# Kernel tuning notes

Measured on AMD Instinct MI355X. Metric: run time of the kernel, lower is better.

The kernel has to match this reference:

```python
import jax, jax.numpy as jnp
import numpy as np

N_NODES = 50000
N_EDGES = 800000
IN_CH, HID_CH, OUT_CH = 100, 128, 47
ORIG_SIZE = 25000


def sage_conv(x, edge_index, w_l, b_l, w_r):
    """PyG-style SAGEConv with mean aggregation.
    out = lin_l(mean_{j in N(i)} x_j) + lin_r(x_i)
    edge_index[0]=source, edge_index[1]=target.
    """
    src, dst = edge_index[0], edge_index[1]
    n = x.shape[0]
    # gather source features, scatter-sum into targets  [N, d]
    agg = jax.ops.segment_sum(x[src], dst, num_segments=n)
    deg = jax.ops.segment_sum(jnp.ones((src.shape[0],), x.dtype), dst, num_segments=n)
    mean = agg / jnp.maximum(deg, 1.0)[:, None]
    return mean @ w_l + b_l + x @ w_r


def setup_inputs() -> dict:
    key = jax.random.key(0)
    ks = jax.random.split(key, 8)
    x = jax.random.normal(ks[0], (N_NODES, IN_CH), dtype=jnp.float32)
    edge_index = jax.random.randint(ks[1], (2, N_EDGES), 0, N_NODES, dtype=jnp.int32)
    s1 = 1.0 / np.sqrt(IN_CH)
    s2 = 1.0 / np.sqrt(HID_CH)
    w1_l = jax.random.uniform(ks[2], (IN_CH, HID_CH), jnp.float32, -s1, s1)
    b1_l = jax.random.uniform(ks[3], (HID_CH,), jnp.float32, -s1, s1)
    w1_r = jax.random.uniform(ks[4], (IN_CH, HID_CH), jnp.float32, -s1, s1)
    w2_l = jax.random.uniform(ks[5], (HID_CH, OUT_CH), jnp.float32, -s2, s2)
    b2_l = jax.random.uniform(ks[6], (OUT_CH,), jnp.float32, -s2, s2)
    w2_r = jax.random.uniform(ks[7], (HID_CH, OUT_CH), jnp.float32, -s2, s2)
    return {"x": x, "edge_index": edge_index, "original_size": ORIG_SIZE,
            "w1_l": w1_l, "b1_l": b1_l, "w1_r": w1_r,
            "w2_l": w2_l, "b2_l": b2_l, "w2_r": w2_r}


def reference(x, edge_index, original_size, w1_l, b1_l, w1_r, w2_l, b2_l, w2_r):
    h = sage_conv(x, edge_index, w1_l, b1_l, w1_r)   # [N, hidden]
    h = sage_conv(h, edge_index, w2_l, b2_l, w2_r)   # [N, out]
    logp = jax.nn.log_softmax(h, axis=1)
    return logp[:original_size]
```

## Files before the change

kernel.cpp:

```cpp
#include <hip/hip_runtime.h>
#include <hip/hip_fp16.h>
#include <math.h>

constexpr int N    = 50000;
constexpr int E    = 800000;
constexpr int CIN  = 100;
constexpr int CH   = 128;
constexpr int COUT = 47;
constexpr int NOUT = 25000;
constexpr int CP   = 48;
constexpr int NB   = (N + 255) / 256;
constexpr int TN   = 128;
constexpr int NT   = (N + TN - 1) / TN;

constexpr int AS  = 72;
constexpr int HS  = 136;
constexpr int W1K = 256;
constexpr int W2K = 128;

constexpr int HB = (E + 255) / 256;
constexpr int CB = (N * CIN / 4 + 255) / 256;
constexpr int PB = 193;

typedef float f32x4 __attribute__((ext_vector_type(4)));
typedef short v8s  __attribute__((ext_vector_type(8)));

__device__ __forceinline__ void bsplit(float f, ushort& h, ushort& l) {
    uint u = __float_as_uint(f);
    h = (ushort)(u >> 16);
    float fh = __uint_as_float(u & 0xffff0000u);
    l = (ushort)(__float_as_uint(f - fh) >> 16);
}

__global__ __launch_bounds__(256) void pre_kernel(
        const int* __restrict__ dst, int* __restrict__ cnt, int* __restrict__ rank,
        const float* __restrict__ x, __half* __restrict__ x16,
        const float* __restrict__ w1l, const float* __restrict__ w1r,
        const float* __restrict__ w2l, const float* __restrict__ w2r,
        const float* __restrict__ b2l,
        ushort* __restrict__ w1T, ushort* __restrict__ w2T,
        float* __restrict__ b2cat) {
    int bid = blockIdx.x, t = threadIdx.x;
    if (bid < HB) {
        int i = bid * 256 + t;
        if (i < E) rank[i] = atomicAdd(&cnt[dst[i]], 1);
    } else if (bid < HB + CB) {
        int i = (bid - HB) * 256 + t;
        if (i < N * CIN / 4) {
            float4 v = ((const float4*)x)[i];
            __half2 h0 = __floats2half2_rn(v.x, v.y);
            __half2 h1 = __floats2half2_rn(v.z, v.w);
            union { __half2 h[2]; uint2 u; } U;
            U.h[0] = h0; U.h[1] = h1;
            ((uint2*)x16)[i] = U.u;
        }
    } else {
        int i = (bid - HB - CB) * 256 + t;
        if (i < 128 * W1K) {
            int n = i >> 8, k = i & 255;
            float v = 0.0f;
            if (k < 100)                    v = w1l[(size_t)k * CH + n];
            else if (k >= 128 && k < 228)   v = w1r[(size_t)(k - 128) * CH + n];
            ushort h, l; bsplit(v, h, l);
            w1T[i] = h; w1T[128 * W1K + i] = l;
        } else if (i < 128 * W1K + 128 * W2K) {
            int j = i - 128 * W1K;
            int n = j >> 7, k = j & 127;
            float v = 0.0f;
            if (n < COUT)                      v = w2l[(size_t)k * COUT + n];
            else if (n >= 64 && n < 64 + COUT) v = w2r[(size_t)k * COUT + (n - 64)];
            ushort h, l; bsplit(v, h, l);
            w2T[j] = h; w2T[128 * W2K + j] = l;
        } else {
            int j = i - (128 * W1K + 128 * W2K);
            if (j < 128) b2cat[j] = (j >= 64 && j < 64 + COUT) ? b2l[j - 64] : 0.0f;
        }
    }
}

__global__ __launch_bounds__(256) void scan_blocks(const int* __restrict__ cnt,
        int* __restrict__ row_ptr, int* __restrict__ blkSum) {
    __shared__ int s[256];
    int t = threadIdx.x;
    int i = blockIdx.x * 256 + t;
    int v = (i < N) ? cnt[i] : 0;
    s[t] = v;
    __syncthreads();
    for (int off = 1; off < 256; off <<= 1) {
        int a = s[t];
        int u = (t >= off) ? s[t - off] : 0;
        __syncthreads();
        s[t] = a + u;
        __syncthreads();
    }
    if (i < N) row_ptr[i] = s[t] - v;
    if (t == 255) blkSum[blockIdx.x] = s[255];
}

__global__ __launch_bounds__(256) void scan_apply(int* __restrict__ row_ptr,
        const int* __restrict__ blkSum) {
    __shared__ int s[256];
    int t = threadIdx.x, bid = blockIdx.x;
    int a = 0;
    for (int j = t; j < bid; j += 256) a += blkSum[j];
    s[t] = a;
    __syncthreads();
    for (int off = 128; off > 0; off >>= 1) {
        if (t < off) s[t] += s[t + off];
        __syncthreads();
    }
    int offset = s[0];
    int i = bid * 256 + t;
    if (i < N) {
        row_ptr[i] += offset;
        if (i == N - 1) row_ptr[N] = E;
    }
}

__global__ void fill_kernel(const int* __restrict__ src, const int* __restrict__ dst,
        const int* __restrict__ rank, const int* __restrict__ row_ptr,
        int* __restrict__ col) {
    int i = blockIdx.x * blockDim.x + threadIdx.x;
    if (i < E) col[row_ptr[dst[i]] + rank[i]] = src[i];
}

__global__ __launch_bounds__(256) void gather1_kernel(const __half* __restrict__ x16,
        const int* __restrict__ row_ptr, const int* __restrict__ col,
        float* __restrict__ agg1) {
    int t = threadIdx.x;
    int n = blockIdx.x * 4 + (t >> 6);
    int l = t & 63, half = l >> 5, li = l & 31;
    int b = row_ptr[n], e = row_ptr[n + 1];
    float inv = 1.0f / (float)max(e - b, 1);
    const uint2* xb = (const uint2*)x16;
    bool act = li < 25;
    float4 s0 = make_float4(0.f, 0.f, 0.f, 0.f);
    float4 s1 = make_float4(0.f, 0.f, 0.f, 0.f);
    float4 s2 = make_float4(0.f, 0.f, 0.f, 0.f);
    float4 s3 = make_float4(0.f, 0.f, 0.f, 0.f);
    union { uint2 u; __half2 h[2]; } U0, U1, U2, U3;
    int j = b + half;
    for (; j + 6 < e; j += 8) {
        int c0 = col[j], c1 = col[j + 2], c2 = col[j + 4], c3 = col[j + 6];
        if (act) {
            U0.u = xb[(size_t)c0 * 25 + li];
            U1.u = xb[(size_t)c1 * 25 + li];
            U2.u = xb[(size_t)c2 * 25 + li];
            U3.u = xb[(size_t)c3 * 25 + li];
            float2 f0a = __half22float2(U0.h[0]), f0b = __half22float2(U0.h[1]);
            float2 f1a = __half22float2(U1.h[0]), f1b = __half22float2(U1.h[1]);
            float2 f2a = __half22float2(U2.h[0]), f2b = __half22float2(U2.h[1]);
            float2 f3a = __half22float2(U3.h[0]), f3b = __half22float2(U3.h[1]);
            s0.x += f0a.x; s0.y += f0a.y; s0.z += f0b.x; s0.w += f0b.y;
            s1.x += f1a.x; s1.y += f1a.y; s1.z += f1b.x; s1.w += f1b.y;
            s2.x += f2a.x; s2.y += f2a.y; s2.z += f2b.x; s2.w += f2b.y;
            s3.x += f3a.x; s3.y += f3a.y; s3.z += f3b.x; s3.w += f3b.y;
        }
    }
    for (; j < e; j += 2) {
        int c0 = col[j];
        if (act) {
            U0.u = xb[(size_t)c0 * 25 + li];
            float2 f0a = __half22float2(U0.h[0]), f0b = __half22float2(U0.h[1]);
            s0.x += f0a.x; s0.y += f0a.y; s0.z += f0b.x; s0.w += f0b.y;
        }
    }
    float4 s = make_float4(s0.x + s1.x + s2.x + s3.x,
                           s0.y + s1.y + s2.y + s3.y,
                           s0.z + s1.z + s2.z + s3.z,
                           s0.w + s1.w + s2.w + s3.w);
    s.x += __shfl_xor(s.x, 32, 64);
    s.y += __shfl_xor(s.y, 32, 64);
    s.z += __shfl_xor(s.z, 32, 64);
    s.w += __shfl_xor(s.w, 32, 64);
    if (half == 0 && act)
        ((float4*)agg1)[(size_t)n * 25 + li] = make_float4(
            s.x * inv, s.y * inv, s.z * inv, s.w * inv);
}

__global__ __launch_bounds__(256) void fused_gemm(
        const float* __restrict__ agg1, const float* __restrict__ x,
        const ushort* __restrict__ w1T, const float* __restrict__ b1l,
        const ushort* __restrict__ w2T, const float* __restrict__ b2cat,
        __half* __restrict__ gsrc16, float* __restrict__ gself) {
    __shared__ __align__(16) uint lds_u[17408];
    ushort* Ah = (ushort*)lds_u;
    ushort* Al = Ah + 128 * AS;
    ushort* Hh = (ushort*)lds_u;
    ushort* Hl = Hh + 128 * HS;

    int t = threadIdx.x;
    int lane = t & 63;
    int wv = __builtin_amdgcn_readfirstlane(t >> 6);
    int nh = wv & 1, chh = wv >> 1;
    int l15 = lane & 15, lg = lane >> 4;
    int base = blockIdx.x * TN;

    const ushort* w1Th = w1T;
    const ushort* w1Tl = w1T + 128 * W1K;
    const ushort* w2Th = w2T;
    const ushort* w2Tl = w2T + 128 * W2K;

    f32x4 acc[4][4];
    #pragma unroll
    for (int nt = 0; nt < 4; ++nt) {
        float bv = b1l[chh * 64 + nt * 16 + l15];
        #pragma unroll
        for (int mt = 0; mt < 4; ++mt)
            acc[mt][nt] = f32x4{bv, bv, bv, bv};
    }

    int srow = t >> 1, sq = t & 1;
    int nmax = N - 1 - base; if (nmax > TN - 1) nmax = TN - 1;
    int srr = srow <= nmax ? srow : nmax;

    float4 rv[8];
    {
        const float4* Fp = (const float4*)(agg1 + (size_t)(base + srr) * CIN);
        int cj0 = sq * 8;
        #pragma unroll
        for (int q = 0; q < 8; ++q) {
            int cj = cj0 + q;
            rv[q] = (cj < 25) ? Fp[cj] : make_float4(0.f, 0.f, 0.f, 0.f);
        }
    }

    for (int c = 0; c < 4; ++c) {
        float4 nv[8];
        if (c < 3) {
            const float* F = (c + 1 < 2) ? agg1 : x;
            const float4* Fp = (const float4*)(F + (size_t)(base + srr) * CIN);
            int cj0 = ((c + 1) & 1) * 16 + sq * 8;
            #pragma unroll
            for (int q = 0; q < 8; ++q) {
                int cj = cj0 + q;
                nv[q] = (cj < 25) ? Fp[cj] : make_float4(0.f, 0.f, 0.f, 0.f);
            }
        }
        #pragma unroll
        for (int q = 0; q < 8; ++q) {
            ushort h0, h1, h2, h3, l0, l1, l2, l3;
            bsplit(rv[q].x, h0, l0); bsplit(rv[q].y, h1, l1);
            bsplit(rv[q].z, h2, l2); bsplit(rv[q].w, h3, l3);
            int di = srow * AS + sq * 32 + q * 4;
            *(uint2*)(Ah + di) = make_uint2((uint)h0 | ((uint)h1 << 16),
                                            (uint)h2 | ((uint)h3 << 16));
            *(uint2*)(Al + di) = make_uint2((uint)l0 | ((uint)l1 << 16),
                                            (uint)l2 | ((uint)l3 << 16));
        }
        __syncthreads();
        #pragma unroll
        for (int ks = 0; ks < 2; ++ks) {
            v8s ahf[4], alf[4];
            #pragma unroll
            for (int mt = 0; mt < 4; ++mt) {
                int row = nh * 64 + mt * 16 + l15;
                int ko = ks * 32 + lg * 8;
                ahf[mt] = *(const v8s*)(Ah + row * AS + ko);
                alf[mt] = *(const v8s*)(Al + row * AS + ko);
            }
            int kg = c * 64 + ks * 32 + lg * 8;
            #pragma unroll
            for (int nt = 0; nt < 4; ++nt) {
                int n = chh * 64 + nt * 16 + l15;
                v8s bhf = *(const v8s*)(w1Th + (size_t)n * W1K + kg);
                v8s blf = *(const v8s*)(w1Tl + (size_t)n * W1K + kg);
                #pragma unroll
                for (int mt = 0; mt < 4; ++mt) {
                    acc[mt][nt] = __builtin_amdgcn_mfma_f32_16x16x32_bf16(
                        ahf[mt], bhf, acc[mt][nt], 0, 0, 0);
                    acc[mt][nt] = __builtin_amdgcn_mfma_f32_16x16x32_bf16(
                        alf[mt], bhf, acc[mt][nt], 0, 0, 0);
                    acc[mt][nt] = __builtin_amdgcn_mfma_f32_16x16x32_bf16(
                        ahf[mt], blf, acc[mt][nt], 0, 0, 0);
                }
            }
        }
        __syncthreads();
        if (c < 3) {
            #pragma unroll
            for (int q = 0; q < 8; ++q) rv[q] = nv[q];
        }
    }

    #pragma unroll
    for (int mt = 0; mt < 4; ++mt) {
        #pragma unroll
        for (int nt = 0; nt < 4; ++nt) {
            int ch = chh * 64 + nt * 16 + l15;
            #pragma unroll
            for (int r = 0; r < 4; ++r) {
                int node = nh * 64 + mt * 16 + lg * 4 + r;
                ushort h, l; bsplit(acc[mt][nt][r], h, l);
                Hh[node * HS + ch] = h;
                Hl[node * HS + ch] = l;
            }
        }
    }
    __syncthreads();

    bool skip = (chh == 1) && (base >= NOUT);
    if (!skip) {
        #pragma unroll
        for (int nt = 0; nt < 4; ++nt) {
            float bv = b2cat[chh * 64 + nt * 16 + l15];
            #pragma unroll
            for (int mt = 0; mt < 4; ++mt)
                acc[mt][nt] = f32x4{bv, bv, bv, bv};
        }
        #pragma unroll
        for (int ks = 0; ks < 4; ++ks) {
            v8s ahf[4], alf[4];
            #pragma unroll
            for (int mt = 0; mt < 4; ++mt) {
                int node = nh * 64 + mt * 16 + l15;
                int ko = ks * 32 + lg * 8;
                ahf[mt] = *(const v8s*)(Hh + node * HS + ko);
                alf[mt] = *(const v8s*)(Hl + node * HS + ko);
            }
            int kg = ks * 32 + lg * 8;
            #pragma unroll
            for (int nt = 0; nt < 4; ++nt) {
                int n = chh * 64 + nt * 16 + l15;
                v8s bhf = *(const v8s*)(w2Th + (size_t)n * W2K + kg);
                v8s blf = *(const v8s*)(w2Tl + (size_t)n * W2K + kg);
                #pragma unroll
                for (int mt = 0; mt < 4; ++mt) {
                    acc[mt][nt] = __builtin_amdgcn_mfma_f32_16x16x32_bf16(
                        ahf[mt], bhf, acc[mt][nt], 0, 0, 0);
                    acc[mt][nt] = __builtin_amdgcn_mfma_f32_16x16x32_bf16(
                        alf[mt], bhf, acc[mt][nt], 0, 0, 0);
                    acc[mt][nt] = __builtin_amdgcn_mfma_f32_16x16x32_bf16(
                        ahf[mt], blf, acc[mt][nt], 0, 0, 0);
                }
            }
        }
        int lim = chh ? NOUT : N;
        #pragma unroll
        for (int nt = 0; nt < 3; ++nt) {
            int colc = nt * 16 + l15;
            #pragma unroll
            for (int mt = 0; mt < 4; ++mt) {
                #pragma unroll
                for (int r = 0; r < 4; ++r) {
                    int node = base + nh * 64 + mt * 16 + lg * 4 + r;
                    if (node < lim) {
                        if (chh) gself[(size_t)node * CP + colc] = acc[mt][nt][r];
                        else gsrc16[(size_t)node * CP + colc] =
                                 __float2half(acc[mt][nt][r]);
                    }
                }
            }
        }
    }
}

__global__ __launch_bounds__(256) void final_kernel(const __half* __restrict__ gsrc16,
        const float* __restrict__ gself, const int* __restrict__ row_ptr,
        const int* __restrict__ col, float* __restrict__ out) {
    int t = threadIdx.x;
    int n = blockIdx.x * 4 + (t >> 6);
    int c = t & 63;
    int b = row_ptr[n], e = row_ptr[n + 1];
    float inv = 1.0f / (float)max(e - b, 1);
    float a0 = 0.f, a1 = 0.f, a2 = 0.f, a3 = 0.f;
    if (c < CP) {
        int j = b;
        for (; j + 3 < e; j += 4) {
            a0 += __half2float(gsrc16[(size_t)col[j]     * CP + c]);
            a1 += __half2float(gsrc16[(size_t)col[j + 1] * CP + c]);
            a2 += __half2float(gsrc16[(size_t)col[j + 2] * CP + c]);
            a3 += __half2float(gsrc16[(size_t)col[j + 3] * CP + c]);
        }
        for (; j < e; ++j) a0 += __half2float(gsrc16[(size_t)col[j] * CP + c]);
    }
    float val = (c < COUT)
        ? (((a0 + a1) + (a2 + a3)) * inv + gself[(size_t)n * CP + c]) : -INFINITY;
    float m = val;
    #pragma unroll
    for (int off = 32; off > 0; off >>= 1) m = fmaxf(m, __shfl_xor(m, off, 64));
    float ex = (c < COUT) ? expf(val - m) : 0.f;
    float ssum = ex;
    #pragma unroll
    for (int off = 32; off > 0; off >>= 1) ssum += __shfl_xor(ssum, off, 64);
    if (c < COUT)
        __builtin_nontemporal_store(val - m - logf(ssum),
                                    out + (size_t)n * COUT + c);
}

extern "C" void kernel_launch(void* const* d_in, const int* in_sizes, int n_in,
                              void* d_out, int out_size, void* d_ws, size_t ws_size,
                              hipStream_t stream) {
    const float* x   = (const float*)d_in[0];
    const int*   ei  = (const int*)d_in[1];
    const int*   src = ei;
    const int*   dst = ei + E;
    const float* w1l = (const float*)d_in[3];
    const float* b1l = (const float*)d_in[4];
    const float* w1r = (const float*)d_in[5];
    const float* w2l = (const float*)d_in[6];
    const float* b2l = (const float*)d_in[7];
    const float* w2r = (const float*)d_in[8];
    float* out = (float*)d_out;

    int* cnt     = (int*)d_ws;
    int* row_ptr = cnt + N;
    int* rank    = row_ptr + N + 1;
    int* blkSum  = rank + E;
    int* col     = blkSum + NB;
    size_t intWords = (size_t)N + (N + 1) + E + NB + E;
    intWords = (intWords + 3) & ~(size_t)3;
    float* agg1   = (float*)d_ws + intWords;
    float* gself  = agg1 + (size_t)N * CIN;
    float* b2cat  = gself + (size_t)NOUT * CP;
    __half* gsrc16 = (__half*)(b2cat + 128);
    __half* x16    = gsrc16 + (size_t)N * CP;
    ushort* w1T   = (ushort*)(x16 + (size_t)N * CIN);
    ushort* w2T   = w1T + 2 * 128 * W1K;

    (void)hipMemsetAsync(cnt, 0, (size_t)N * sizeof(int), stream);
    pre_kernel  <<<HB + CB + PB, 256, 0, stream>>>(dst, cnt, rank, x, x16,
                                                   w1l, w1r, w2l, w2r, b2l,
                                                   w1T, w2T, b2cat);
    scan_blocks <<<NB, 256, 0, stream>>>(cnt, row_ptr, blkSum);
    scan_apply  <<<NB, 256, 0, stream>>>(row_ptr, blkSum);
    fill_kernel <<<(E + 255) / 256, 256, 0, stream>>>(src, dst, rank, row_ptr, col);
    gather1_kernel<<<N / 4, 256, 0, stream>>>(x16, row_ptr, col, agg1);
    fused_gemm  <<<NT, 256, 0, stream>>>(agg1, x, w1T, b1l, w2T, b2cat, gsrc16, gself);
    final_kernel<<<NOUT / 4, 256, 0, stream>>>(gsrc16, gself, row_ptr, col, out);
}
```

Before: 231.1 us.

## Compute x@W1r inside the gather kernel and store aggregates in fp16

Moves the self-term GEMM x@w1_r into extra blocks of the gather kernel, so it runs concurrently with the latency-bound neighbor gather. The result goes to an fp16 buffer that the fused GEMM adds to its accumulator. The aggregated means are also stored in fp16 instead of fp32, which halves that traffic and lets the fused GEMM do only two K-chunks instead of four. In exchange it adds an extra 50000x128 fp16 write and read, plus fp16 rounding on the aggregates and on the x@W partial sums.

```diff
diff --git a/kernel.cpp b/kernel.cpp
--- a/kernel.cpp
+++ b/kernel.cpp
@@ -21,6 +21,8 @@
 constexpr int HB = (E + 255) / 256;
 constexpr int CB = (N * CIN / 4 + 255) / 256;
 constexpr int PB = 193;
+constexpr int XWB = NT;
+constexpr int GB  = N / 4;
 
 typedef float f32x4 __attribute__((ext_vector_type(4)));
 typedef short v8s  __attribute__((ext_vector_type(8)));
@@ -124,11 +126,83 @@
     if (i < E) col[row_ptr[dst[i]] + rank[i]] = src[i];
 }
 
-__global__ __launch_bounds__(256) void gather1_kernel(const __half* __restrict__ x16,
+__global__ __launch_bounds__(256) void gather1_xw(const __half* __restrict__ x16,
         const int* __restrict__ row_ptr, const int* __restrict__ col,
-        float* __restrict__ agg1) {
+        __half* __restrict__ agg1h,
+        const float* __restrict__ x, const ushort* __restrict__ w1T,
+        __half* __restrict__ xw) {
     int t = threadIdx.x;
-    int n = blockIdx.x * 4 + (t >> 6);
+    if (blockIdx.x < XWB) {
+        int base = blockIdx.x * TN;
+        int lane = t & 63;
+        int wv = __builtin_amdgcn_readfirstlane(t >> 6);
+        int nh = wv & 1, chh = wv >> 1;
+        int l15 = lane & 15, lg = lane >> 4;
+        const ushort* w1Th = w1T;
+        const ushort* w1Tl = w1T + 128 * W1K;
+        f32x4 acc[4][4];
+        #pragma unroll
+        for (int mt = 0; mt < 4; ++mt)
+            #pragma unroll
+            for (int nt = 0; nt < 4; ++nt) acc[mt][nt] = f32x4{0.f, 0.f, 0.f, 0.f};
+        #pragma unroll
+        for (int ks = 0; ks < 4; ++ks) {
+            int k0 = ks * 32 + lg * 8;
+            v8s ahf[4], alf[4];
+            #pragma unroll
+            for (int mt = 0; mt < 4; ++mt) {
+                int row = base + nh * 64 + mt * 16 + l15;
+                int rr = row < N ? row : N - 1;
+                const float* xr = x + (size_t)rr * CIN;
+                float4 va = (k0 < 100)
+                    ? *(const float4*)(xr + k0) : make_float4(0.f, 0.f, 0.f, 0.f);
+                float4 vb = (k0 + 4 < 100)
+                    ? *(const float4*)(xr + k0 + 4) : make_float4(0.f, 0.f, 0.f, 0.f);
+                ushort h0, h1, h2, h3, h4, h5, h6, h7;
+                ushort l0, l1, l2, l3, l4, l5, l6, l7;
+                bsplit(va.x, h0, l0); bsplit(va.y, h1, l1);
+                bsplit(va.z, h2, l2); bsplit(va.w, h3, l3);
+                bsplit(vb.x, h4, l4); bsplit(vb.y, h5, l5);
+                bsplit(vb.z, h6, l6); bsplit(vb.w, h7, l7);
+                v8s ah = {(short)h0, (short)h1, (short)h2, (short)h3,
+                          (short)h4, (short)h5, (short)h6, (short)h7};
+                v8s al = {(short)l0, (short)l1, (short)l2, (short)l3,
+                          (short)l4, (short)l5, (short)l6, (short)l7};
+                ahf[mt] = ah; alf[mt] = al;
+            }
+            int kgx = 128 + k0;
+            #pragma unroll
+            for (int nt = 0; nt < 4; ++nt) {
+                int n = chh * 64 + nt * 16 + l15;
+                v8s bhf = *(const v8s*)(w1Th + (size_t)n * W1K + kgx);
+                v8s blf = *(const v8s*)(w1Tl + (size_t)n * W1K + kgx);
+                #pragma unroll
+                for (int mt = 0; mt < 4; ++mt) {
+                    acc[mt][nt] = __builtin_amdgcn_mfma_f32_16x16x32_bf16(
+                        ahf[mt], bhf, acc[mt][nt], 0, 0, 0);
+                    acc[mt][nt] = __builtin_amdgcn_mfma_f32_16x16x32_bf16(
+                        alf[mt], bhf, acc[mt][nt], 0, 0, 0);
+                    acc[mt][nt] = __builtin_amdgcn_mfma_f32_16x16x32_bf16(
+                        ahf[mt], blf, acc[mt][nt], 0, 0, 0);
+                }
+            }
+        }
+        #pragma unroll
+        for (int nt = 0; nt < 4; ++nt) {
+            int ch = chh * 64 + nt * 16 + l15;
+            #pragma unroll
+            for (int mt = 0; mt < 4; ++mt) {
+                #pragma unroll
+                for (int r = 0; r < 4; ++r) {
+                    int node = base + nh * 64 + mt * 16 + lg * 4 + r;
+                    if (node < N)
+                        xw[(size_t)node * 128 + ch] = __float2half(acc[mt][nt][r]);
+                }
+            }
+        }
+        return;
+    }
+    int n = (blockIdx.x - XWB) * 4 + (t >> 6);
     int l = t & 63, half = l >> 5, li = l & 31;
     int b = row_ptr[n], e = row_ptr[n + 1];
     float inv = 1.0f / (float)max(e - b, 1);
@@ -173,13 +247,17 @@
     s.y += __shfl_xor(s.y, 32, 64);
     s.z += __shfl_xor(s.z, 32, 64);
     s.w += __shfl_xor(s.w, 32, 64);
-    if (half == 0 && act)
-        ((float4*)agg1)[(size_t)n * 25 + li] = make_float4(
-            s.x * inv, s.y * inv, s.z * inv, s.w * inv);
+    if (half == 0 && act) {
+        __half2 p0 = __floats2half2_rn(s.x * inv, s.y * inv);
+        __half2 p1 = __floats2half2_rn(s.z * inv, s.w * inv);
+        union { __half2 h[2]; uint2 u; } P;
+        P.h[0] = p0; P.h[1] = p1;
+        ((uint2*)agg1h)[(size_t)n * 25 + li] = P.u;
+    }
 }
 
 __global__ __launch_bounds__(256) void fused_gemm(
-        const float* __restrict__ agg1, const float* __restrict__ x,
+        const __half* __restrict__ agg1h, const __half* __restrict__ xw,
         const ushort* __restrict__ w1T, const float* __restrict__ b1l,
         const ushort* __restrict__ w2T, const float* __restrict__ b2cat,
         __half* __restrict__ gsrc16, float* __restrict__ gself) {
@@ -213,35 +291,29 @@
     int srow = t >> 1, sq = t & 1;
     int nmax = N - 1 - base; if (nmax > TN - 1) nmax = TN - 1;
     int srr = srow <= nmax ? srow : nmax;
-
-    float4 rv[8];
-    {
-        const float4* Fp = (const float4*)(agg1 + (size_t)(base + srr) * CIN);
-        int cj0 = sq * 8;
+    const uint2* Fp = (const uint2*)(agg1h + (size_t)(base + srr) * CIN);
+
+    uint2 rv[8];
+    #pragma unroll
+    for (int q = 0; q < 8; ++q) rv[q] = Fp[sq * 8 + q];
+
+    for (int c = 0; c < 2; ++c) {
+        uint2 nv[8];
+        if (c == 0) {
+            #pragma unroll
+            for (int q = 0; q < 8; ++q) {
+                int cj = 16 + sq * 8 + q;
+                nv[q] = (cj < 25) ? Fp[cj] : make_uint2(0u, 0u);
+            }
+        }
         #pragma unroll
         for (int q = 0; q < 8; ++q) {
-            int cj = cj0 + q;
-            rv[q] = (cj < 25) ? Fp[cj] : make_float4(0.f, 0.f, 0.f, 0.f);
-        }
-    }
-
-    for (int c = 0; c < 4; ++c) {
-        float4 nv[8];
-        if (c < 3) {
-            const float* F = (c + 1 < 2) ? agg1 : x;
-            const float4* Fp = (const float4*)(F + (size_t)(base + srr) * CIN);
-            int cj0 = ((c + 1) & 1) * 16 + sq * 8;
-            #pragma unroll
-            for (int q = 0; q < 8; ++q) {
-                int cj = cj0 + q;
-                nv[q] = (cj < 25) ? Fp[cj] : make_float4(0.f, 0.f, 0.f, 0.f);
-            }
-        }
-        #pragma unroll
-        for (int q = 0; q < 8; ++q) {
+            union { uint2 u; __half2 h[2]; } V; V.u = rv[q];
+            float2 fa = __half22float2(V.h[0]);
+            float2 fb = __half22float2(V.h[1]);
             ushort h0, h1, h2, h3, l0, l1, l2, l3;
-            bsplit(rv[q].x, h0, l0); bsplit(rv[q].y, h1, l1);
-            bsplit(rv[q].z, h2, l2); bsplit(rv[q].w, h3, l3);
+            bsplit(fa.x, h0, l0); bsplit(fa.y, h1, l1);
+            bsplit(fb.x, h2, l2); bsplit(fb.y, h3, l3);
             int di = srow * AS + sq * 32 + q * 4;
             *(uint2*)(Ah + di) = make_uint2((uint)h0 | ((uint)h1 << 16),
                                             (uint)h2 | ((uint)h3 << 16));
@@ -277,9 +349,23 @@
             }
         }
         __syncthreads();
-        if (c < 3) {
+        if (c == 0) {
             #pragma unroll
             for (int q = 0; q < 8; ++q) rv[q] = nv[q];
+        }
+    }
+
+    #pragma unroll
+    for (int mt = 0; mt < 4; ++mt) {
+        #pragma unroll
+        for (int nt = 0; nt < 4; ++nt) {
+            int ch = chh * 64 + nt * 16 + l15;
+            #pragma unroll
+            for (int r = 0; r < 4; ++r) {
+                int node = base + nh * 64 + mt * 16 + lg * 4 + r;
+                if (node < N)
+                    acc[mt][nt][r] += __half2float(xw[(size_t)node * 128 + ch]);
+            }
         }
     }
 
@@ -410,12 +496,13 @@
     int* col     = blkSum + NB;
     size_t intWords = (size_t)N + (N + 1) + E + NB + E;
     intWords = (intWords + 3) & ~(size_t)3;
-    float* agg1   = (float*)d_ws + intWords;
-    float* gself  = agg1 + (size_t)N * CIN;
+    float* gself  = (float*)d_ws + intWords;
     float* b2cat  = gself + (size_t)NOUT * CP;
     __half* gsrc16 = (__half*)(b2cat + 128);
     __half* x16    = gsrc16 + (size_t)N * CP;
-    ushort* w1T   = (ushort*)(x16 + (size_t)N * CIN);
+    __half* agg1h  = x16 + (size_t)N * CIN;
+    __half* xw     = agg1h + (size_t)N * CIN;
+    ushort* w1T   = (ushort*)(xw + (size_t)N * 128);
     ushort* w2T   = w1T + 2 * 128 * W1K;
 
     (void)hipMemsetAsync(cnt, 0, (size_t)N * sizeof(int), stream);
@@ -425,7 +512,9 @@
     scan_blocks <<<NB, 256, 0, stream>>>(cnt, row_ptr, blkSum);
     scan_apply  <<<NB, 256, 0, stream>>>(row_ptr, blkSum);
     fill_kernel <<<(E + 255) / 256, 256, 0, stream>>>(src, dst, rank, row_ptr, col);
-    gather1_kernel<<<N / 4, 256, 0, stream>>>(x16, row_ptr, col, agg1);
-    fused_gemm  <<<NT, 256, 0, stream>>>(agg1, x, w1T, b1l, w2T, b2cat, gsrc16, gself);
+    gather1_xw  <<<XWB + GB, 256, 0, stream>>>(x16, row_ptr, col, agg1h,
+                                               x, w1T, xw);
+    fused_gemm  <<<NT, 256, 0, stream>>>(agg1h, xw, w1T, b1l, w2T, b2cat,
+                                         gsrc16, gself);
     final_kernel<<<NOUT / 4, 256, 0, stream>>>(gsrc16, gself, row_ptr, col, out);
 }
```

Result: slower. 299.3 us (+29.5%).

## Store layer-1 GEMM input as padded fp16 concat and read MFMA fragments directly

Applied to the files above, without the earlier changes.

The mean aggregate and the x copy are now written as fp16 into one zero-padded [N,256] buffer: the aggregate goes into the first 128 columns and x into the upper half. The first GEMM then loads MFMA A-fragments straight from global memory and splits them into bf16 hi/lo in registers, so the LDS staging, bsplit stores and barriers are gone. This halves the traffic for the intermediate aggregate and removes synchronisation. In exchange the aggregate is rounded to fp16, which loses precision, and each wave issues uncoalesced row-strided global loads that may hit memory again instead of sharing through LDS.

```diff
diff --git a/kernel.cpp b/kernel.cpp
--- a/kernel.cpp
+++ b/kernel.cpp
@@ -13,13 +13,13 @@
 constexpr int TN   = 128;
 constexpr int NT   = (N + TN - 1) / TN;
 
-constexpr int AS  = 72;
 constexpr int HS  = 136;
 constexpr int W1K = 256;
 constexpr int W2K = 128;
+constexpr int A1S = 256;
 
 constexpr int HB = (E + 255) / 256;
-constexpr int CB = (N * CIN / 4 + 255) / 256;
+constexpr int CB = (N * 32) / 256;
 constexpr int PB = 193;
 
 typedef float f32x4 __attribute__((ext_vector_type(4)));
@@ -32,9 +32,25 @@
     l = (ushort)(__float_as_uint(f - fh) >> 16);
 }
 
+__device__ __forceinline__ void unpack8(uint4 v, v8s& ah, v8s& al) {
+    union { uint4 u; __half2 h[4]; } V; V.u = v;
+    ushort hh[8], ll[8];
+    #pragma unroll
+    for (int p = 0; p < 4; ++p) {
+        float2 f = __half22float2(V.h[p]);
+        bsplit(f.x, hh[2 * p],     ll[2 * p]);
+        bsplit(f.y, hh[2 * p + 1], ll[2 * p + 1]);
+    }
+    ah = v8s{(short)hh[0], (short)hh[1], (short)hh[2], (short)hh[3],
+             (short)hh[4], (short)hh[5], (short)hh[6], (short)hh[7]};
+    al = v8s{(short)ll[0], (short)ll[1], (short)ll[2], (short)ll[3],
+             (short)ll[4], (short)ll[5], (short)ll[6], (short)ll[7]};
+}
+
 __global__ __launch_bounds__(256) void pre_kernel(
         const int* __restrict__ dst, int* __restrict__ cnt, int* __restrict__ rank,
         const float* __restrict__ x, __half* __restrict__ x16,
+        __half* __restrict__ a1x,
         const float* __restrict__ w1l, const float* __restrict__ w1r,
         const float* __restrict__ w2l, const float* __restrict__ w2r,
         const float* __restrict__ b2l,
@@ -45,15 +61,19 @@
         int i = bid * 256 + t;
         if (i < E) rank[i] = atomicAdd(&cnt[dst[i]], 1);
     } else if (bid < HB + CB) {
-        int i = (bid - HB) * 256 + t;
-        if (i < N * CIN / 4) {
-            float4 v = ((const float4*)x)[i];
+        int j = (bid - HB) * 256 + t;
+        int row = j >> 5, s = j & 31;
+        uint2 u = make_uint2(0u, 0u);
+        if (s < 25) {
+            float4 v = ((const float4*)x)[row * 25 + s];
             __half2 h0 = __floats2half2_rn(v.x, v.y);
             __half2 h1 = __floats2half2_rn(v.z, v.w);
             union { __half2 h[2]; uint2 u; } U;
             U.h[0] = h0; U.h[1] = h1;
-            ((uint2*)x16)[i] = U.u;
-        }
+            u = U.u;
+            ((uint2*)x16)[row * 25 + s] = u;
+        }
+        ((uint2*)a1x)[(size_t)row * 64 + 32 + s] = u;
     } else {
         int i = (bid - HB - CB) * 256 + t;
         if (i < 128 * W1K) {
@@ -64,16 +84,16 @@
             ushort h, l; bsplit(v, h, l);
             w1T[i] = h; w1T[128 * W1K + i] = l;
         } else if (i < 128 * W1K + 128 * W2K) {
-            int j = i - 128 * W1K;
-            int n = j >> 7, k = j & 127;
+            int j2 = i - 128 * W1K;
+            int n = j2 >> 7, k = j2 & 127;
             float v = 0.0f;
             if (n < COUT)                      v = w2l[(size_t)k * COUT + n];
             else if (n >= 64 && n < 64 + COUT) v = w2r[(size_t)k * COUT + (n - 64)];
             ushort h, l; bsplit(v, h, l);
-            w2T[j] = h; w2T[128 * W2K + j] = l;
+            w2T[j2] = h; w2T[128 * W2K + j2] = l;
         } else {
-            int j = i - (128 * W1K + 128 * W2K);
-            if (j < 128) b2cat[j] = (j >= 64 && j < 64 + COUT) ? b2l[j - 64] : 0.0f;
+            int j2 = i - (128 * W1K + 128 * W2K);
+            if (j2 < 128) b2cat[j2] = (j2 >= 64 && j2 < 64 + COUT) ? b2l[j2 - 64] : 0.0f;
         }
     }
 }
@@ -126,7 +146,7 @@
 
 __global__ __launch_bounds__(256) void gather1_kernel(const __half* __restrict__ x16,
         const int* __restrict__ row_ptr, const int* __restrict__ col,
-        float* __restrict__ agg1) {
+        __half* __restrict__ a1x) {
     int t = threadIdx.x;
     int n = blockIdx.x * 4 + (t >> 6);
     int l = t & 63, half = l >> 5, li = l & 31;
@@ -173,19 +193,21 @@
     s.y += __shfl_xor(s.y, 32, 64);
     s.z += __shfl_xor(s.z, 32, 64);
     s.w += __shfl_xor(s.w, 32, 64);
-    if (half == 0 && act)
-        ((float4*)agg1)[(size_t)n * 25 + li] = make_float4(
-            s.x * inv, s.y * inv, s.z * inv, s.w * inv);
+    if (half == 0) {
+        __half2 p0 = __floats2half2_rn(s.x * inv, s.y * inv);
+        __half2 p1 = __floats2half2_rn(s.z * inv, s.w * inv);
+        union { __half2 h[2]; uint2 u; } P;
+        P.h[0] = p0; P.h[1] = p1;
+        ((uint2*)a1x)[(size_t)n * 64 + li] = P.u;
+    }
 }
 
 __global__ __launch_bounds__(256) void fused_gemm(
-        const float* __restrict__ agg1, const float* __restrict__ x,
+        const __half* __restrict__ a1x,
         const ushort* __restrict__ w1T, const float* __restrict__ b1l,
         const ushort* __restrict__ w2T, const float* __restrict__ b2cat,
         __half* __restrict__ gsrc16, float* __restrict__ gself) {
     __shared__ __align__(16) uint lds_u[17408];
-    ushort* Ah = (ushort*)lds_u;
-    ushort* Al = Ah + 128 * AS;
     ushort* Hh = (ushort*)lds_u;
     ushort* Hl = Hh + 128 * HS;
 
@@ -210,76 +232,31 @@
             acc[mt][nt] = f32x4{bv, bv, bv, bv};
     }
 
-    int srow = t >> 1, sq = t & 1;
-    int nmax = N - 1 - base; if (nmax > TN - 1) nmax = TN - 1;
-    int srr = srow <= nmax ? srow : nmax;
-
-    float4 rv[8];
-    {
-        const float4* Fp = (const float4*)(agg1 + (size_t)(base + srr) * CIN);
-        int cj0 = sq * 8;
-        #pragma unroll
-        for (int q = 0; q < 8; ++q) {
-            int cj = cj0 + q;
-            rv[q] = (cj < 25) ? Fp[cj] : make_float4(0.f, 0.f, 0.f, 0.f);
-        }
-    }
-
-    for (int c = 0; c < 4; ++c) {
-        float4 nv[8];
-        if (c < 3) {
-            const float* F = (c + 1 < 2) ? agg1 : x;
-            const float4* Fp = (const float4*)(F + (size_t)(base + srr) * CIN);
-            int cj0 = ((c + 1) & 1) * 16 + sq * 8;
-            #pragma unroll
-            for (int q = 0; q < 8; ++q) {
-                int cj = cj0 + q;
-                nv[q] = (cj < 25) ? Fp[cj] : make_float4(0.f, 0.f, 0.f, 0.f);
+    #pragma unroll 2
+    for (int ks = 0; ks < 8; ++ks) {
+        int k0 = ks * 32 + lg * 8;
+        v8s ahf[4], alf[4];
+        #pragma unroll
+        for (int mt = 0; mt < 4; ++mt) {
+            int row = base + nh * 64 + mt * 16 + l15;
+            int rr = row < N ? row : N - 1;
+            uint4 v = *(const uint4*)(a1x + (size_t)rr * A1S + k0);
+            unpack8(v, ahf[mt], alf[mt]);
+        }
+        #pragma unroll
+        for (int nt = 0; nt < 4; ++nt) {
+            int n = chh * 64 + nt * 16 + l15;
+            v8s bhf = *(const v8s*)(w1Th + (size_t)n * W1K + k0);
+            v8s blf = *(const v8s*)(w1Tl + (size_t)n * W1K + k0);
+            #pragma unroll
+            for (int mt = 0; mt < 4; ++mt) {
+                acc[mt][nt] = __builtin_amdgcn_mfma_f32_16x16x32_bf16(
+                    ahf[mt], bhf, acc[mt][nt], 0, 0, 0);
+                acc[mt][nt] = __builtin_amdgcn_mfma_f32_16x16x32_bf16(
+                    alf[mt], bhf, acc[mt][nt], 0, 0, 0);
+                acc[mt][nt] = __builtin_amdgcn_mfma_f32_16x16x32_bf16(
+                    ahf[mt], blf, acc[mt][nt], 0, 0, 0);
             }
-        }
-        #pragma unroll
-        for (int q = 0; q < 8; ++q) {
-            ushort h0, h1, h2, h3, l0, l1, l2, l3;
-            bsplit(rv[q].x, h0, l0); bsplit(rv[q].y, h1, l1);
-            bsplit(rv[q].z, h2, l2); bsplit(rv[q].w, h3, l3);
-            int di = srow * AS + sq * 32 + q * 4;
-            *(uint2*)(Ah + di) = make_uint2((uint)h0 | ((uint)h1 << 16),
-                                            (uint)h2 | ((uint)h3 << 16));
-            *(uint2*)(Al + di) = make_uint2((uint)l0 | ((uint)l1 << 16),
-                                            (uint)l2 | ((uint)l3 << 16));
-        }
-        __syncthreads();
-        #pragma unroll
-        for (int ks = 0; ks < 2; ++ks) {
-            v8s ahf[4], alf[4];
-            #pragma unroll
-            for (int mt = 0; mt < 4; ++mt) {
-                int row = nh * 64 + mt * 16 + l15;
-                int ko = ks * 32 + lg * 8;
-                ahf[mt] = *(const v8s*)(Ah + row * AS + ko);
-                alf[mt] = *(const v8s*)(Al + row * AS + ko);
-            }
-            int kg = c * 64 + ks * 32 + lg * 8;
-            #pragma unroll
-            for (int nt = 0; nt < 4; ++nt) {
-                int n = chh * 64 + nt * 16 + l15;
-                v8s bhf = *(const v8s*)(w1Th + (size_t)n * W1K + kg);
-                v8s blf = *(const v8s*)(w1Tl + (size_t)n * W1K + kg);
-                #pragma unroll
-                for (int mt = 0; mt < 4; ++mt) {
-                    acc[mt][nt] = __builtin_amdgcn_mfma_f32_16x16x32_bf16(
-                        ahf[mt], bhf, acc[mt][nt], 0, 0, 0);
-                    acc[mt][nt] = __builtin_amdgcn_mfma_f32_16x16x32_bf16(
-                        alf[mt], bhf, acc[mt][nt], 0, 0, 0);
-                    acc[mt][nt] = __builtin_amdgcn_mfma_f32_16x16x32_bf16(
-                        ahf[mt], blf, acc[mt][nt], 0, 0, 0);
-                }
-            }
-        }
-        __syncthreads();
-        if (c < 3) {
-            #pragma unroll
-            for (int q = 0; q < 8; ++q) rv[q] = nv[q];
         }
     }
 
@@ -410,22 +387,23 @@
     int* col     = blkSum + NB;
     size_t intWords = (size_t)N + (N + 1) + E + NB + E;
     intWords = (intWords + 3) & ~(size_t)3;
-    float* agg1   = (float*)d_ws + intWords;
-    float* gself  = agg1 + (size_t)N * CIN;
+    float* gself  = (float*)d_ws + intWords;
     float* b2cat  = gself + (size_t)NOUT * CP;
     __half* gsrc16 = (__half*)(b2cat + 128);
     __half* x16    = gsrc16 + (size_t)N * CP;
-    ushort* w1T   = (ushort*)(x16 + (size_t)N * CIN);
+    __half* a1x    = x16 + (size_t)N * CIN;
+    ushort* w1T   = (ushort*)(a1x + (size_t)N * A1S);
     ushort* w2T   = w1T + 2 * 128 * W1K;
 
     (void)hipMemsetAsync(cnt, 0, (size_t)N * sizeof(int), stream);
-    pre_kernel  <<<HB + CB + PB, 256, 0, stream>>>(dst, cnt, rank, x, x16,
+    pre_kernel  <<<HB + CB + PB, 256, 0, stream>>>(dst, cnt, rank, x, x16, a1x,
                                                    w1l, w1r, w2l, w2r, b2l,
                                                    w1T, w2T, b2cat);
     scan_blocks <<<NB, 256, 0, stream>>>(cnt, row_ptr, blkSum);
     scan_apply  <<<NB, 256, 0, stream>>>(row_ptr, blkSum);
     fill_kernel <<<(E + 255) / 256, 256, 0, stream>>>(src, dst, rank, row_ptr, col);
-    gather1_kernel<<<N / 4, 256, 0, stream>>>(x16, row_ptr, col, agg1);
-    fused_gemm  <<<NT, 256, 0, stream>>>(agg1, x, w1T, b1l, w2T, b2cat, gsrc16, gself);
+    gather1_kernel<<<N / 4, 256, 0, stream>>>(x16, row_ptr, col, a1x);
+    fused_gemm  <<<NT, 256, 0, stream>>>(a1x, w1T, b1l, w2T, b2cat,
+                                         gsrc16, gself);
     final_kernel<<<NOUT / 4, 256, 0, stream>>>(gsrc16, gself, row_ptr, col, out);
 }
```

After: 227.2 us. About the same (-1.7%).
